# Kernel tuning notes

Hardware: AMD Instinct MI355X
Metric: run time of the kernel (lower is better)

The kernel has to match this reference:

```python
import jax, jax.numpy as jnp
import numpy as np

EMBED_DIM = 1024
NUM_HEADS = 16
HEAD_DIM = EMBED_DIM // NUM_HEADS
N, S = 4, 2048


def setup_inputs() -> dict:
    key = jax.random.key(0)
    ks = jax.random.split(key, 11)
    s = 1.0 / np.sqrt(EMBED_DIM)
    inp = {
        'query': jax.random.normal(ks[0], (N, S, EMBED_DIM), jnp.float32),
        'key': jax.random.normal(ks[1], (N, S, EMBED_DIM), jnp.float32),
        'value': jax.random.normal(ks[2], (N, S, EMBED_DIM), jnp.float32),
        'wq': jax.random.normal(ks[3], (EMBED_DIM, EMBED_DIM), jnp.float32) * s,
        'bq': jnp.zeros((EMBED_DIM,), jnp.float32),
        'wk': jax.random.normal(ks[4], (EMBED_DIM, EMBED_DIM), jnp.float32) * s,
        'bk': jnp.zeros((EMBED_DIM,), jnp.float32),
        'wv': jax.random.normal(ks[5], (EMBED_DIM, EMBED_DIM), jnp.float32) * s,
        'bv': jnp.zeros((EMBED_DIM,), jnp.float32),
        'wo': jax.random.normal(ks[6], (EMBED_DIM, EMBED_DIM), jnp.float32) * s,
        'bo': jnp.zeros((EMBED_DIM,), jnp.float32),
    }
    return inp


def reference(query, key, value, wq, bq, wk, bk, wv, bv, wo, bo):
    n = query.shape[0]
    # projections: y = x @ W^T + b (torch nn.Linear convention)
    Q = query @ wq.T + bq
    K = key @ wk.T + bk
    V = value @ wv.T + bv
    # [n, h, s, d]
    Q = Q.reshape(n, -1, NUM_HEADS, HEAD_DIM).transpose(0, 2, 1, 3)
    K = K.reshape(n, -1, NUM_HEADS, HEAD_DIM).transpose(0, 2, 1, 3)
    V = V.reshape(n, -1, NUM_HEADS, HEAD_DIM).transpose(0, 2, 1, 3)
    energy = jnp.einsum('nhqd,nhkd->nhqk', Q, K)
    attn = jax.nn.softmax(energy / jnp.sqrt(jnp.float32(HEAD_DIM)), axis=-1)
    out = jnp.einsum('nhqk,nhkd->nhqd', attn, V)
    out = out.transpose(0, 2, 1, 3).reshape(n, -1, NUM_HEADS * HEAD_DIM)
    return out @ wo.T + bo
```

## Files before the change

kernel.cpp:

```cpp
#include <hip/hip_runtime.h>
#include <hip/hip_bf16.h>

#define EMBED 1024
#define SEQ   2048
#define NB    4
#define NH    16
#define HD    64
#define MROWS (NB*SEQ)
#define WELEM (EMBED*EMBED)

typedef __attribute__((ext_vector_type(4))) float  f32x4;
typedef __attribute__((ext_vector_type(8))) short  s16x8;

#define MFMA16(a,b,c) __builtin_amdgcn_mfma_f32_16x16x32_bf16((a),(b),(c),0,0,0)

__device__ __forceinline__ unsigned short f2bf(float f) {
    union { float f; unsigned int u; } v; v.f = f;
    unsigned int r = v.u + 0x7fffu + ((v.u >> 16) & 1u);
    return (unsigned short)(r >> 16);
}
__device__ __forceinline__ unsigned int cvtpk(float a, float b) {
    unsigned int r;
    asm("v_cvt_pk_bf16_f32 %0, %1, %2" : "=v"(r) : "v"(a), "v"(b));
    return r;
}
__device__ __forceinline__ float exp2r(float x) {
    float r;
    asm("v_exp_f32 %0, %1" : "=v"(r) : "v"(x));
    return r;
}
__device__ __forceinline__ void gload16(const void* g, void* l) {
    __builtin_amdgcn_global_load_lds(
        (const __attribute__((address_space(1))) void*)g,
        (__attribute__((address_space(3))) void*)l, 16, 0, 0);
}

#define SC2 0.18033688f

__global__ __launch_bounds__(256) void conv_w(
    const float* __restrict__ wq, const float* __restrict__ wk,
    const float* __restrict__ wv, const float* __restrict__ wo,
    unsigned short* __restrict__ Wbf)
{
    const int i   = blockIdx.x*256 + threadIdx.x;
    const int seg = i >> 17;
    const int off = i & 131071;
    const float* src = seg == 0 ? wq : (seg == 1 ? wk : (seg == 2 ? wv : wo));
    const float sc   = seg == 0 ? SC2 : 1.f;
    const float4 a = *(const float4*)(src + (size_t)off*8);
    const float4 b = *(const float4*)(src + (size_t)off*8 + 4);
    uint4 o;
    o.x = cvtpk(a.x*sc, a.y*sc); o.y = cvtpk(a.z*sc, a.w*sc);
    o.z = cvtpk(b.x*sc, b.y*sc); o.w = cvtpk(b.z*sc, b.w*sc);
    *(uint4*)(Wbf + (size_t)seg*WELEM + (size_t)off*8) = o;
}

template<int WMODE>
__global__ __launch_bounds__(256) void qkv_fused(
    const float* __restrict__ Aq, const float* __restrict__ Ak,
    const float* __restrict__ Av,
    const float* __restrict__ wq, const float* __restrict__ wk,
    const float* __restrict__ wv, const unsigned short* __restrict__ Wbf,
    const float* __restrict__ bq, const float* __restrict__ bk,
    const float* __restrict__ bv,
    unsigned short* __restrict__ Qp, unsigned short* __restrict__ Kp,
    unsigned short* __restrict__ Vt)
{
    __shared__ unsigned short Ald[128*72];
    __shared__ unsigned short Bld[WMODE ? 128*64 : 128*72];
    const int t    = threadIdx.x;
    const int i    = blockIdx.x;
    const int work = (i & 7)*192 + (i >> 3);
    const int bm   = work / 24;
    const int bnq  = work % 24;
    const int sel  = bnq >> 3, bnl = bnq & 7;
    const float* Af   = sel == 0 ? Aq : (sel == 1 ? Ak : Av);
    const float* Wf   = sel == 0 ? wq : (sel == 1 ? wk : wv);
    const unsigned short* Wb = Wbf + (size_t)sel*WELEM;
    const float* bias = sel == 0 ? bq : (sel == 1 ? bk : bv);

    const int wid = t >> 6, lane = t & 63, l15 = lane & 15, blk = lane >> 4;
    const int wr  = wid >> 1, wc = wid & 1;

    f32x4 acc[4][4] = {};

    for (int kt = 0; kt < EMBED/64; ++kt) {
        if (WMODE == 1) {
            #pragma unroll
            for (int j = 0; j < 4; ++j) {
                const int u = j*256 + t, row = u >> 3, slot = u & 7;
                const unsigned short* src = Wb + (size_t)(bnl*128+row)*EMBED
                                               + kt*64 + (slot ^ (row & 7))*8;
                gload16(src, (char*)Bld + j*4096 + wid*1024);
            }
        }
        #pragma unroll
        for (int j = 0; j < 8; ++j) {
            int f = t + 256*j, row = f >> 4, c4 = f & 15;
            float4 v = *(const float4*)(Af + (size_t)(bm*128+row)*EMBED + kt*64 + c4*4);
            *(uint2*)&Ald[row*72 + c4*4] = make_uint2(cvtpk(v.x,v.y), cvtpk(v.z,v.w));
        }
        if (WMODE == 0) {
            #pragma unroll
            for (int j = 0; j < 8; ++j) {
                int f = t + 256*j, row = f >> 4, c4 = f & 15;
                float4 v = *(const float4*)(Wf + (size_t)(bnl*128+row)*EMBED + kt*64 + c4*4);
                *(uint2*)&Bld[row*72 + c4*4] = make_uint2(cvtpk(v.x,v.y), cvtpk(v.z,v.w));
            }
        } else {
            asm volatile("s_waitcnt vmcnt(0)" ::: "memory");
        }
        __syncthreads();
        #pragma unroll
        for (int ks = 0; ks < 2; ++ks) {
            s16x8 af[4], bf[4];
            #pragma unroll
            for (int mt = 0; mt < 4; ++mt)
                af[mt] = *(const s16x8*)&Ald[(wr*64 + mt*16 + l15)*72 + ks*32 + blk*8];
            #pragma unroll
            for (int nt = 0; nt < 4; ++nt) {
                const int rb = wc*64 + nt*16 + l15;
                if (WMODE == 1)
                    bf[nt] = *(const s16x8*)((const char*)Bld + rb*128
                                 + ((ks*64 + blk*16) ^ ((rb & 7) << 4)));
                else
                    bf[nt] = *(const s16x8*)&Bld[rb*72 + ks*32 + blk*8];
            }
            #pragma unroll
            for (int mt = 0; mt < 4; ++mt)
                #pragma unroll
                for (int nt = 0; nt < 4; ++nt)
                    acc[mt][nt] = MFMA16(af[mt], bf[nt], acc[mt][nt]);
        }
        __syncthreads();
    }

    const float scale = (sel == 0) ? SC2 : 1.0f;
    float bv4[4];
    #pragma unroll
    for (int nt = 0; nt < 4; ++nt) {
        float bb = bias[bnl*128 + wc*64 + nt*16 + l15];
        bv4[nt] = (WMODE == 1) ? bb*scale : bb;
    }

    #pragma unroll
    for (int mt = 0; mt < 4; ++mt) {
        #pragma unroll
        for (int nt = 0; nt < 4; ++nt) {
            const int m0 = bm*128 + wr*64 + mt*16 + blk*4;
            const int n  = bnl*128 + wc*64 + nt*16 + l15;
            f32x4 a = acc[mt][nt];
            if (sel < 2) {
                unsigned short* Yb = (sel == 0) ? Qp : Kp;
                #pragma unroll
                for (int r = 0; r < 4; ++r) {
                    float val = (WMODE == 1) ? (a[r] + bv4[nt])
                                             : (a[r] + bv4[nt]) * scale;
                    Yb[(size_t)(m0+r)*EMBED + n] = f2bf(val);
                }
            } else {
                const int b = m0 >> 11, s = m0 & (SEQ-1);
                const int h = n >> 6,  d = n & (HD-1);
                ushort4 pk;
                pk.x = f2bf(a[0] + bv4[nt]); pk.y = f2bf(a[1] + bv4[nt]);
                pk.z = f2bf(a[2] + bv4[nt]); pk.w = f2bf(a[3] + bv4[nt]);
                *(ushort4*)&Vt[(((size_t)b*NH + h)*HD + d)*SEQ + s] = pk;
            }
        }
    }
}

template<int WMODE>
__global__ __launch_bounds__(256) void gemm_out(
    const unsigned short* __restrict__ Ab, const float* __restrict__ W,
    const unsigned short* __restrict__ Wb,
    const float* __restrict__ bias, float* __restrict__ Yf)
{
    __shared__ unsigned short Ald[128*64];
    __shared__ unsigned short Bld[WMODE ? 128*64 : 128*72];
    const int t    = threadIdx.x;
    const int i    = blockIdx.x;
    const int work = (i & 7)*64 + (i >> 3);
    const int bm   = work >> 3;
    const int bn   = work & 7;
    const int wid = t >> 6, lane = t & 63, l15 = lane & 15, blk = lane >> 4;
    const int wr  = wid >> 1, wc = wid & 1;

    f32x4 acc[4][4] = {};

    for (int kt = 0; kt < EMBED/64; ++kt) {
        #pragma unroll
        for (int j = 0; j < 4; ++j) {
            const int u = j*256 + t, row = u >> 3, slot = u & 7;
            const unsigned short* src = Ab + (size_t)(bm*128+row)*EMBED
                                           + kt*64 + (slot ^ (row & 7))*8;
            gload16(src, (char*)Ald + j*4096 + wid*1024);
        }
        if (WMODE == 1) {
            #pragma unroll
            for (int j = 0; j < 4; ++j) {
                const int u = j*256 + t, row = u >> 3, slot = u & 7;
                const unsigned short* src = Wb + (size_t)(bn*128+row)*EMBED
                                               + kt*64 + (slot ^ (row & 7))*8;
                gload16(src, (char*)Bld + j*4096 + wid*1024);
            }
        } else {
            #pragma unroll
            for (int j = 0; j < 8; ++j) {
                int f = t + 256*j, row = f >> 4, c4 = f & 15;
                float4 v = *(const float4*)(W + (size_t)(bn*128+row)*EMBED + kt*64 + c4*4);
                *(uint2*)&Bld[row*72 + c4*4] = make_uint2(cvtpk(v.x,v.y), cvtpk(v.z,v.w));
            }
        }
        asm volatile("s_waitcnt vmcnt(0)" ::: "memory");
        __syncthreads();
        #pragma unroll
        for (int ks = 0; ks < 2; ++ks) {
            s16x8 af[4], bf[4];
            #pragma unroll
            for (int mt = 0; mt < 4; ++mt) {
                const int ra = wr*64 + mt*16 + l15;
                af[mt] = *(const s16x8*)((const char*)Ald + ra*128
                             + ((ks*64 + blk*16) ^ ((ra & 7) << 4)));
            }
            #pragma unroll
            for (int nt = 0; nt < 4; ++nt) {
                const int rb = wc*64 + nt*16 + l15;
                if (WMODE == 1)
                    bf[nt] = *(const s16x8*)((const char*)Bld + rb*128
                                 + ((ks*64 + blk*16) ^ ((rb & 7) << 4)));
                else
                    bf[nt] = *(const s16x8*)&Bld[rb*72 + ks*32 + blk*8];
            }
            #pragma unroll
            for (int mt = 0; mt < 4; ++mt)
                #pragma unroll
                for (int nt = 0; nt < 4; ++nt)
                    acc[mt][nt] = MFMA16(af[mt], bf[nt], acc[mt][nt]);
        }
        __syncthreads();
    }

    float bv4[4];
    #pragma unroll
    for (int nt = 0; nt < 4; ++nt)
        bv4[nt] = bias[bn*128 + wc*64 + nt*16 + l15];

    #pragma unroll
    for (int mt = 0; mt < 4; ++mt)
        #pragma unroll
        for (int nt = 0; nt < 4; ++nt) {
            const int m0 = bm*128 + wr*64 + mt*16 + blk*4;
            const int n  = bn*128 + wc*64 + nt*16 + l15;
            f32x4 a = acc[mt][nt];
            #pragma unroll
            for (int r = 0; r < 4; ++r)
                Yf[(size_t)(m0+r)*EMBED + n] = a[r] + bv4[nt];
        }
}

__global__ __launch_bounds__(512) void attn_fwd(
    const unsigned short* __restrict__ Qp,
    const unsigned short* __restrict__ Kp,
    const unsigned short* __restrict__ Vt,
    unsigned short* __restrict__ ctx)
{
    __shared__ unsigned short Kld[2][64*64];
    __shared__ unsigned short Vld[2][64*64];
    __shared__ unsigned short Pld[8][32*64];

    const int t = threadIdx.x, wid = t >> 6, lane = t & 63;
    const int l15 = lane & 15, blk = lane >> 4;
    const int bh = blockIdx.x, qb = blockIdx.y;
    const int b = bh >> 4, h = bh & (NH-1);
    const int q0 = qb*256 + wid*32;

    s16x8 qf[2][2];
    #pragma unroll
    for (int qs = 0; qs < 2; ++qs) {
        const unsigned short* qp = Qp + (size_t)(b*SEQ + q0 + qs*16 + l15)*EMBED + h*HD;
        qf[qs][0] = *(const s16x8*)(qp + blk*8);
        qf[qs][1] = *(const s16x8*)(qp + 32 + blk*8);
    }

    const unsigned short* kb = Kp + (size_t)b*SEQ*EMBED + h*HD;
    const unsigned short* vb = Vt + (size_t)bh*HD*SEQ;

    const int u  = wid*64 + lane;
    const int r0 = u >> 3;
    const int s0 = ((((u&7)<<4) ^ ((r0&7)<<4)) >> 1);
    const unsigned short* kS = kb + (size_t)r0*EMBED + s0;
    const unsigned short* vS = vb + (size_t)r0*SEQ  + s0;

    unsigned short* pl = &Pld[wid][0];
    const int rc0 = (blk*16) ^ ((l15 & 7) << 4);
    const int rc1 = rc0 ^ 64;

    s16x8 onesf;
    #pragma unroll
    for (int j = 0; j < 8; ++j) onesf[j] = (short)0x3F80;

    f32x4 o[2][4] = {};
    f32x4 sacc[2] = {};

    gload16(kS, (char*)Kld[0] + wid*1024);
    gload16(vS, (char*)Vld[0] + wid*1024);
    asm volatile("s_waitcnt vmcnt(0)" ::: "memory");
    __syncthreads();

    int cur = 0;
    for (int tt = 0; tt < SEQ/64; ++tt) {
        if (tt + 1 < SEQ/64) {
            const size_t ko = (size_t)(tt+1)*64;
            gload16(kS + ko*EMBED, (char*)Kld[cur^1] + wid*1024);
            gload16(vS + ko,       (char*)Vld[cur^1] + wid*1024);
        }

        const char* kbase = (const char*)Kld[cur];
        const char* vbase = (const char*)Vld[cur];

        f32x4 sc[2][4];
        #pragma unroll
        for (int qs = 0; qs < 2; ++qs)
            #pragma unroll
            for (int kt = 0; kt < 4; ++kt)
                sc[qs][kt] = f32x4{0.f,0.f,0.f,0.f};
        __builtin_amdgcn_s_setprio(1);
        #pragma unroll
        for (int kt = 0; kt < 4; ++kt) {
            const char* krow = kbase + (kt*16 + l15)*128;
            s16x8 ka0 = *(const s16x8*)(krow + rc0);
            s16x8 ka1 = *(const s16x8*)(krow + rc1);
            #pragma unroll
            for (int qs = 0; qs < 2; ++qs) {
                sc[qs][kt] = MFMA16(ka0, qf[qs][0], sc[qs][kt]);
                sc[qs][kt] = MFMA16(ka1, qf[qs][1], sc[qs][kt]);
            }
        }
        __builtin_amdgcn_s_setprio(0);

        #pragma unroll
        for (int qs = 0; qs < 2; ++qs) {
            #pragma unroll
            for (int kt = 0; kt < 4; ++kt) {
                const float e0 = exp2r(sc[qs][kt][0]);
                const float e1 = exp2r(sc[qs][kt][1]);
                const float e2 = exp2r(sc[qs][kt][2]);
                const float e3 = exp2r(sc[qs][kt][3]);
                const int off = (qs*16 + l15)*128 + ((kt*32 + blk*8) ^ ((l15 & 7) << 4));
                *(uint2*)((char*)pl + off) = make_uint2(cvtpk(e0,e1), cvtpk(e2,e3));
            }
        }

        s16x8 pa[2][2];
        #pragma unroll
        for (int qs = 0; qs < 2; ++qs) {
            const char* prow = (const char*)pl + (qs*16 + l15)*128;
            pa[qs][0] = *(const s16x8*)(prow + rc0);
            pa[qs][1] = *(const s16x8*)(prow + rc1);
        }
        __builtin_amdgcn_s_setprio(1);
        #pragma unroll
        for (int qs = 0; qs < 2; ++qs) {
            sacc[qs] = MFMA16(pa[qs][0], onesf, sacc[qs]);
            sacc[qs] = MFMA16(pa[qs][1], onesf, sacc[qs]);
        }
        #pragma unroll
        for (int dt = 0; dt < 4; ++dt) {
            const char* vrow = vbase + (dt*16 + l15)*128;
            s16x8 vb0 = *(const s16x8*)(vrow + rc0);
            s16x8 vb1 = *(const s16x8*)(vrow + rc1);
            #pragma unroll
            for (int qs = 0; qs < 2; ++qs) {
                o[qs][dt] = MFMA16(pa[qs][0], vb0, o[qs][dt]);
                o[qs][dt] = MFMA16(pa[qs][1], vb1, o[qs][dt]);
            }
        }
        __builtin_amdgcn_s_setprio(0);

        asm volatile("s_waitcnt vmcnt(0)" ::: "memory");
        __syncthreads();
        cur ^= 1;
    }

    #pragma unroll
    for (int qs = 0; qs < 2; ++qs) {
        float li[4];
        #pragma unroll
        for (int r = 0; r < 4; ++r) li[r] = 1.f / sacc[qs][r];
        unsigned short* cp = ctx + (size_t)(b*SEQ + q0 + qs*16)*EMBED + h*HD;
        #pragma unroll
        for (int dt = 0; dt < 4; ++dt)
            #pragma unroll
            for (int r = 0; r < 4; ++r)
                cp[(size_t)(blk*4 + r)*EMBED + dt*16 + l15] = f2bf(o[qs][dt][r] * li[r]);
    }
}

extern "C" void kernel_launch(void* const* d_in, const int* in_sizes, int n_in,
                              void* d_out, int out_size, void* d_ws, size_t ws_size,
                              hipStream_t stream)
{
    const float* q  = (const float*)d_in[0];
    const float* k  = (const float*)d_in[1];
    const float* v  = (const float*)d_in[2];
    const float* wq = (const float*)d_in[3];
    const float* bq = (const float*)d_in[4];
    const float* wk = (const float*)d_in[5];
    const float* bk = (const float*)d_in[6];
    const float* wv = (const float*)d_in[7];
    const float* bv = (const float*)d_in[8];
    const float* wo = (const float*)d_in[9];
    const float* bo = (const float*)d_in[10];

    unsigned short* Qp  = (unsigned short*)d_out;
    unsigned short* Kp  = Qp + (size_t)MROWS*EMBED;
    unsigned short* Vt  = (unsigned short*)d_ws;
    unsigned short* ctx = Vt + (size_t)MROWS*EMBED;
    unsigned short* Wbf = ctx + (size_t)MROWS*EMBED;
    float* out = (float*)d_out;

    const bool pre = ws_size >= (size_t)40*1024*1024;

    dim3 tpb(256);
    if (pre) {
        conv_w<<<2048, tpb, 0, stream>>>(wq, wk, wv, wo, Wbf);
        qkv_fused<1><<<1536, tpb, 0, stream>>>(
            q, k, v, wq, wk, wv, Wbf, bq, bk, bv, Qp, Kp, Vt);
    } else {
        qkv_fused<0><<<1536, tpb, 0, stream>>>(
            q, k, v, wq, wk, wv, Wbf, bq, bk, bv, Qp, Kp, Vt);
    }
    attn_fwd<<<dim3(NB*NH, SEQ/256), dim3(512), 0, stream>>>(Qp, Kp, Vt, ctx);
    if (pre) {
        gemm_out<1><<<512, tpb, 0, stream>>>(
            ctx, wo, Wbf + (size_t)3*WELEM, bo, out);
    } else {
        gemm_out<0><<<512, tpb, 0, stream>>>(
            ctx, wo, Wbf, bo, out);
    }
}
```

Baseline: 183.1 us.

## Software-pipeline QKV loads, enlarge attention per-wave query tile, use 2D grids

The QKV GEMM (pre-converted weight path) now prefetches the next fp32 activation tile into registers while the current one is converted and multiplied, so global loads overlap with compute. The attention kernel drops from 512 to 256 threads, and each wave now handles 64 query rows instead of 32, reusing K fragments across four query subtiles. Both GEMMs switch from a swizzled 1D block ordering to a plain 2D grid. In exchange, register pressure rises in both kernels, attention has fewer waves per block to hide latency, and the L2-friendly block ordering is lost.

```diff
diff --git a/kernel.cpp b/kernel.cpp
--- a/kernel.cpp
+++ b/kernel.cpp
@@ -68,12 +68,9 @@
 {
     __shared__ unsigned short Ald[128*72];
     __shared__ unsigned short Bld[WMODE ? 128*64 : 128*72];
-    const int t    = threadIdx.x;
-    const int i    = blockIdx.x;
-    const int work = (i & 7)*192 + (i >> 3);
-    const int bm   = work / 24;
-    const int bnq  = work % 24;
-    const int sel  = bnq >> 3, bnl = bnq & 7;
+    const int t   = threadIdx.x;
+    const int bm  = blockIdx.x, bn = blockIdx.y;
+    const int sel = bn >> 3, bnl = bn & 7;
     const float* Af   = sel == 0 ? Aq : (sel == 1 ? Ak : Av);
     const float* Wf   = sel == 0 ? wq : (sel == 1 ? wk : wv);
     const unsigned short* Wb = Wbf + (size_t)sel*WELEM;
@@ -84,55 +81,101 @@
 
     f32x4 acc[4][4] = {};
 
-    for (int kt = 0; kt < EMBED/64; ++kt) {
-        if (WMODE == 1) {
-            #pragma unroll
-            for (int j = 0; j < 4; ++j) {
-                const int u = j*256 + t, row = u >> 3, slot = u & 7;
-                const unsigned short* src = Wb + (size_t)(bnl*128+row)*EMBED
-                                               + kt*64 + (slot ^ (row & 7))*8;
-                gload16(src, (char*)Bld + j*4096 + wid*1024);
-            }
-        }
-        #pragma unroll
-        for (int j = 0; j < 8; ++j) {
-            int f = t + 256*j, row = f >> 4, c4 = f & 15;
-            float4 v = *(const float4*)(Af + (size_t)(bm*128+row)*EMBED + kt*64 + c4*4);
-            *(uint2*)&Ald[row*72 + c4*4] = make_uint2(cvtpk(v.x,v.y), cvtpk(v.z,v.w));
-        }
-        if (WMODE == 0) {
+#define QKV_LOADW(ktc)                                                        \
+    _Pragma("unroll")                                                         \
+    for (int j = 0; j < 4; ++j) {                                             \
+        const int u = j*256 + t, row = u >> 3, slot = u & 7;                  \
+        gload16(Wb + (size_t)(bnl*128+row)*EMBED + (ktc)*64                   \
+                   + (slot ^ (row & 7))*8,                                    \
+                (char*)Bld + j*4096 + wid*1024);                              \
+    }
+#define QKV_LOADA(dst, ktc)                                                   \
+    _Pragma("unroll")                                                         \
+    for (int j = 0; j < 8; ++j) {                                             \
+        int f = t + 256*j, row = f >> 4, c4 = f & 15;                         \
+        dst[j] = *(const float4*)(Af + (size_t)(bm*128+row)*EMBED             \
+                                     + (ktc)*64 + c4*4);                      \
+    }
+#define QKV_CONVA(src)                                                        \
+    _Pragma("unroll")                                                         \
+    for (int j = 0; j < 8; ++j) {                                             \
+        int f = t + 256*j, row = f >> 4, c4 = f & 15;                         \
+        *(uint2*)&Ald[row*72 + c4*4] =                                        \
+            make_uint2(cvtpk(src[j].x,src[j].y), cvtpk(src[j].z,src[j].w));   \
+    }
+#define QKV_MFMAS()                                                           \
+    _Pragma("unroll")                                                         \
+    for (int ks = 0; ks < 2; ++ks) {                                          \
+        s16x8 af[4], bf[4];                                                   \
+        _Pragma("unroll")                                                     \
+        for (int mt = 0; mt < 4; ++mt)                                        \
+            af[mt] = *(const s16x8*)&Ald[(wr*64 + mt*16 + l15)*72             \
+                                         + ks*32 + blk*8];                    \
+        _Pragma("unroll")                                                     \
+        for (int nt = 0; nt < 4; ++nt) {                                      \
+            const int rb = wc*64 + nt*16 + l15;                               \
+            bf[nt] = *(const s16x8*)((const char*)Bld + rb*128                \
+                         + ((ks*64 + blk*16) ^ ((rb & 7) << 4)));             \
+        }                                                                     \
+        _Pragma("unroll")                                                     \
+        for (int mt = 0; mt < 4; ++mt)                                        \
+            _Pragma("unroll")                                                 \
+            for (int nt = 0; nt < 4; ++nt)                                    \
+                acc[mt][nt] = MFMA16(af[mt], bf[nt], acc[mt][nt]);            \
+    }
+
+    if (WMODE == 1) {
+        float4 arA[8], arB[8];
+        QKV_LOADA(arA, 0);
+        for (int kt = 0; kt < 16; kt += 2) {
+            QKV_LOADW(kt);
+            QKV_LOADA(arB, kt+1);
+            QKV_CONVA(arA);
+            asm volatile("s_waitcnt vmcnt(8)" ::: "memory");
+            __syncthreads();
+            QKV_MFMAS();
+            __syncthreads();
+            QKV_LOADW(kt+1);
+            if (kt + 2 < 16) { QKV_LOADA(arA, kt+2); }
+            QKV_CONVA(arB);
+            if (kt + 2 < 16) { asm volatile("s_waitcnt vmcnt(8)" ::: "memory"); }
+            else             { asm volatile("s_waitcnt vmcnt(0)" ::: "memory"); }
+            __syncthreads();
+            QKV_MFMAS();
+            __syncthreads();
+        }
+    } else {
+        for (int kt = 0; kt < 16; ++kt) {
+            #pragma unroll
+            for (int j = 0; j < 8; ++j) {
+                int f = t + 256*j, row = f >> 4, c4 = f & 15;
+                float4 v = *(const float4*)(Af + (size_t)(bm*128+row)*EMBED + kt*64 + c4*4);
+                *(uint2*)&Ald[row*72 + c4*4] = make_uint2(cvtpk(v.x,v.y), cvtpk(v.z,v.w));
+            }
             #pragma unroll
             for (int j = 0; j < 8; ++j) {
                 int f = t + 256*j, row = f >> 4, c4 = f & 15;
                 float4 v = *(const float4*)(Wf + (size_t)(bnl*128+row)*EMBED + kt*64 + c4*4);
                 *(uint2*)&Bld[row*72 + c4*4] = make_uint2(cvtpk(v.x,v.y), cvtpk(v.z,v.w));
             }
-        } else {
-            asm volatile("s_waitcnt vmcnt(0)" ::: "memory");
-        }
-        __syncthreads();
-        #pragma unroll
-        for (int ks = 0; ks < 2; ++ks) {
-            s16x8 af[4], bf[4];
-            #pragma unroll
-            for (int mt = 0; mt < 4; ++mt)
-                af[mt] = *(const s16x8*)&Ald[(wr*64 + mt*16 + l15)*72 + ks*32 + blk*8];
-            #pragma unroll
-            for (int nt = 0; nt < 4; ++nt) {
-                const int rb = wc*64 + nt*16 + l15;
-                if (WMODE == 1)
-                    bf[nt] = *(const s16x8*)((const char*)Bld + rb*128
-                                 + ((ks*64 + blk*16) ^ ((rb & 7) << 4)));
-                else
-                    bf[nt] = *(const s16x8*)&Bld[rb*72 + ks*32 + blk*8];
-            }
-            #pragma unroll
-            for (int mt = 0; mt < 4; ++mt)
+            __syncthreads();
+            #pragma unroll
+            for (int ks = 0; ks < 2; ++ks) {
+                s16x8 af[4], bf[4];
+                #pragma unroll
+                for (int mt = 0; mt < 4; ++mt)
+                    af[mt] = *(const s16x8*)&Ald[(wr*64 + mt*16 + l15)*72 + ks*32 + blk*8];
                 #pragma unroll
                 for (int nt = 0; nt < 4; ++nt)
-                    acc[mt][nt] = MFMA16(af[mt], bf[nt], acc[mt][nt]);
-        }
-        __syncthreads();
+                    bf[nt] = *(const s16x8*)&Bld[(wc*64 + nt*16 + l15)*72 + ks*32 + blk*8];
+                #pragma unroll
+                for (int mt = 0; mt < 4; ++mt)
+                    #pragma unroll
+                    for (int nt = 0; nt < 4; ++nt)
+                        acc[mt][nt] = MFMA16(af[mt], bf[nt], acc[mt][nt]);
+            }
+            __syncthreads();
+        }
     }
 
     const float scale = (sel == 0) ? SC2 : 1.0f;
@@ -178,11 +221,8 @@
 {
     __shared__ unsigned short Ald[128*64];
     __shared__ unsigned short Bld[WMODE ? 128*64 : 128*72];
-    const int t    = threadIdx.x;
-    const int i    = blockIdx.x;
-    const int work = (i & 7)*64 + (i >> 3);
-    const int bm   = work >> 3;
-    const int bn   = work & 7;
+    const int t   = threadIdx.x;
+    const int bm  = blockIdx.x, bn = blockIdx.y;
     const int wid = t >> 6, lane = t & 63, l15 = lane & 15, blk = lane >> 4;
     const int wr  = wid >> 1, wc = wid & 1;
 
@@ -259,7 +299,7 @@
         }
 }
 
-__global__ __launch_bounds__(512) void attn_fwd(
+__global__ __launch_bounds__(256) void attn_fwd(
     const unsigned short* __restrict__ Qp,
     const unsigned short* __restrict__ Kp,
     const unsigned short* __restrict__ Vt,
@@ -267,17 +307,17 @@
 {
     __shared__ unsigned short Kld[2][64*64];
     __shared__ unsigned short Vld[2][64*64];
-    __shared__ unsigned short Pld[8][32*64];
+    __shared__ unsigned short Pld[4][64*64];
 
     const int t = threadIdx.x, wid = t >> 6, lane = t & 63;
     const int l15 = lane & 15, blk = lane >> 4;
     const int bh = blockIdx.x, qb = blockIdx.y;
     const int b = bh >> 4, h = bh & (NH-1);
-    const int q0 = qb*256 + wid*32;
-
-    s16x8 qf[2][2];
-    #pragma unroll
-    for (int qs = 0; qs < 2; ++qs) {
+    const int q0 = qb*256 + wid*64;
+
+    s16x8 qf[4][2];
+    #pragma unroll
+    for (int qs = 0; qs < 4; ++qs) {
         const unsigned short* qp = Qp + (size_t)(b*SEQ + q0 + qs*16 + l15)*EMBED + h*HD;
         qf[qs][0] = *(const s16x8*)(qp + blk*8);
         qf[qs][1] = *(const s16x8*)(qp + 32 + blk*8);
@@ -286,11 +326,15 @@
     const unsigned short* kb = Kp + (size_t)b*SEQ*EMBED + h*HD;
     const unsigned short* vb = Vt + (size_t)bh*HD*SEQ;
 
-    const int u  = wid*64 + lane;
-    const int r0 = u >> 3;
-    const int s0 = ((((u&7)<<4) ^ ((r0&7)<<4)) >> 1);
-    const unsigned short* kS = kb + (size_t)r0*EMBED + s0;
-    const unsigned short* vS = vb + (size_t)r0*SEQ  + s0;
+    const int c0 = wid*2, c1 = wid*2 + 1;
+    const int u0 = c0*64 + lane,              u1 = c1*64 + lane;
+    const int r0 = u0 >> 3,                   r1 = u1 >> 3;
+    const int s0 = ((((u0&7)<<4) ^ ((r0&7)<<4)) >> 1);
+    const int s1 = ((((u1&7)<<4) ^ ((r1&7)<<4)) >> 1);
+    const unsigned short* kS0 = kb + (size_t)r0*EMBED + s0;
+    const unsigned short* kS1 = kb + (size_t)r1*EMBED + s1;
+    const unsigned short* vS0 = vb + (size_t)r0*SEQ  + s0;
+    const unsigned short* vS1 = vb + (size_t)r1*SEQ  + s1;
 
     unsigned short* pl = &Pld[wid][0];
     const int rc0 = (blk*16) ^ ((l15 & 7) << 4);
@@ -300,11 +344,13 @@
     #pragma unroll
     for (int j = 0; j < 8; ++j) onesf[j] = (short)0x3F80;
 
-    f32x4 o[2][4] = {};
-    f32x4 sacc[2] = {};
-
-    gload16(kS, (char*)Kld[0] + wid*1024);
-    gload16(vS, (char*)Vld[0] + wid*1024);
+    f32x4 o[4][4] = {};
+    f32x4 sacc[4] = {};
+
+    gload16(kS0, (char*)Kld[0] + c0*1024);
+    gload16(kS1, (char*)Kld[0] + c1*1024);
+    gload16(vS0, (char*)Vld[0] + c0*1024);
+    gload16(vS1, (char*)Vld[0] + c1*1024);
     asm volatile("s_waitcnt vmcnt(0)" ::: "memory");
     __syncthreads();
 
@@ -312,56 +358,55 @@
     for (int tt = 0; tt < SEQ/64; ++tt) {
         if (tt + 1 < SEQ/64) {
             const size_t ko = (size_t)(tt+1)*64;
-            gload16(kS + ko*EMBED, (char*)Kld[cur^1] + wid*1024);
-            gload16(vS + ko,       (char*)Vld[cur^1] + wid*1024);
+            char* kd = (char*)Kld[cur^1];
+            char* vd = (char*)Vld[cur^1];
+            gload16(kS0 + ko*EMBED, kd + c0*1024);
+            gload16(kS1 + ko*EMBED, kd + c1*1024);
+            gload16(vS0 + ko,       vd + c0*1024);
+            gload16(vS1 + ko,       vd + c1*1024);
         }
 
         const char* kbase = (const char*)Kld[cur];
         const char* vbase = (const char*)Vld[cur];
 
-        f32x4 sc[2][4];
-        #pragma unroll
-        for (int qs = 0; qs < 2; ++qs)
-            #pragma unroll
-            for (int kt = 0; kt < 4; ++kt)
-                sc[qs][kt] = f32x4{0.f,0.f,0.f,0.f};
-        __builtin_amdgcn_s_setprio(1);
+        s16x8 ka[4][2];
         #pragma unroll
         for (int kt = 0; kt < 4; ++kt) {
             const char* krow = kbase + (kt*16 + l15)*128;
-            s16x8 ka0 = *(const s16x8*)(krow + rc0);
-            s16x8 ka1 = *(const s16x8*)(krow + rc1);
-            #pragma unroll
-            for (int qs = 0; qs < 2; ++qs) {
-                sc[qs][kt] = MFMA16(ka0, qf[qs][0], sc[qs][kt]);
-                sc[qs][kt] = MFMA16(ka1, qf[qs][1], sc[qs][kt]);
-            }
-        }
-        __builtin_amdgcn_s_setprio(0);
-
-        #pragma unroll
-        for (int qs = 0; qs < 2; ++qs) {
+            ka[kt][0] = *(const s16x8*)(krow + rc0);
+            ka[kt][1] = *(const s16x8*)(krow + rc1);
+        }
+
+        #pragma unroll
+        for (int qs = 0; qs < 4; ++qs) {
+            f32x4 sc[4];
+            #pragma unroll
+            for (int kt = 0; kt < 4; ++kt) sc[kt] = f32x4{0.f,0.f,0.f,0.f};
+            __builtin_amdgcn_s_setprio(1);
             #pragma unroll
             for (int kt = 0; kt < 4; ++kt) {
-                const float e0 = exp2r(sc[qs][kt][0]);
-                const float e1 = exp2r(sc[qs][kt][1]);
-                const float e2 = exp2r(sc[qs][kt][2]);
-                const float e3 = exp2r(sc[qs][kt][3]);
+                sc[kt] = MFMA16(ka[kt][0], qf[qs][0], sc[kt]);
+                sc[kt] = MFMA16(ka[kt][1], qf[qs][1], sc[kt]);
+            }
+            __builtin_amdgcn_s_setprio(0);
+            #pragma unroll
+            for (int kt = 0; kt < 4; ++kt) {
+                const float e0 = exp2r(sc[kt][0]);
+                const float e1 = exp2r(sc[kt][1]);
+                const float e2 = exp2r(sc[kt][2]);
+                const float e3 = exp2r(sc[kt][3]);
                 const int off = (qs*16 + l15)*128 + ((kt*32 + blk*8) ^ ((l15 & 7) << 4));
                 *(uint2*)((char*)pl + off) = make_uint2(cvtpk(e0,e1), cvtpk(e2,e3));
             }
         }
 
-        s16x8 pa[2][2];
-        #pragma unroll
-        for (int qs = 0; qs < 2; ++qs) {
+        s16x8 pa[4][2];
+        __builtin_amdgcn_s_setprio(1);
+        #pragma unroll
+        for (int qs = 0; qs < 4; ++qs) {
             const char* prow = (const char*)pl + (qs*16 + l15)*128;
             pa[qs][0] = *(const s16x8*)(prow + rc0);
             pa[qs][1] = *(const s16x8*)(prow + rc1);
-        }
-        __builtin_amdgcn_s_setprio(1);
-        #pragma unroll
-        for (int qs = 0; qs < 2; ++qs) {
             sacc[qs] = MFMA16(pa[qs][0], onesf, sacc[qs]);
             sacc[qs] = MFMA16(pa[qs][1], onesf, sacc[qs]);
         }
@@ -371,7 +416,7 @@
             s16x8 vb0 = *(const s16x8*)(vrow + rc0);
             s16x8 vb1 = *(const s16x8*)(vrow + rc1);
             #pragma unroll
-            for (int qs = 0; qs < 2; ++qs) {
+            for (int qs = 0; qs < 4; ++qs) {
                 o[qs][dt] = MFMA16(pa[qs][0], vb0, o[qs][dt]);
                 o[qs][dt] = MFMA16(pa[qs][1], vb1, o[qs][dt]);
             }
@@ -384,7 +429,7 @@
     }
 
     #pragma unroll
-    for (int qs = 0; qs < 2; ++qs) {
+    for (int qs = 0; qs < 4; ++qs) {
         float li[4];
         #pragma unroll
         for (int r = 0; r < 4; ++r) li[r] = 1.f / sacc[qs][r];
@@ -425,18 +470,18 @@
     dim3 tpb(256);
     if (pre) {
         conv_w<<<2048, tpb, 0, stream>>>(wq, wk, wv, wo, Wbf);
-        qkv_fused<1><<<1536, tpb, 0, stream>>>(
+        qkv_fused<1><<<dim3(MROWS/128, 24), tpb, 0, stream>>>(
             q, k, v, wq, wk, wv, Wbf, bq, bk, bv, Qp, Kp, Vt);
     } else {
-        qkv_fused<0><<<1536, tpb, 0, stream>>>(
+        qkv_fused<0><<<dim3(MROWS/128, 24), tpb, 0, stream>>>(
             q, k, v, wq, wk, wv, Wbf, bq, bk, bv, Qp, Kp, Vt);
     }
-    attn_fwd<<<dim3(NB*NH, SEQ/256), dim3(512), 0, stream>>>(Qp, Kp, Vt, ctx);
+    attn_fwd<<<dim3(NB*NH, SEQ/256), tpb, 0, stream>>>(Qp, Kp, Vt, ctx);
     if (pre) {
-        gemm_out<1><<<512, tpb, 0, stream>>>(
+        gemm_out<1><<<dim3(MROWS/128, EMBED/128), tpb, 0, stream>>>(
             ctx, wo, Wbf + (size_t)3*WELEM, bo, out);
     } else {
-        gemm_out<0><<<512, tpb, 0, stream>>>(
+        gemm_out<0><<<dim3(MROWS/128, EMBED/128), tpb, 0, stream>>>(
             ctx, wo, Wbf, bo, out);
     }
 }
```

Measured after the change: 256.7 us. 1.4x slower.
